# Performance work log

Hardware: AMD Instinct MI355X
Metric: run time of the kernel (lower is better)

The kernel has to match this reference:

```python
import jax, jax.numpy as jnp
import numpy as np

NUM_NODES = 50000
NUM_EDGES = 800000
IN_CH = 128
OUT_CH = 128


def setup_inputs() -> dict:
    key = jax.random.key(0)
    k1, k2, k3 = jax.random.split(key, 3)
    x = jax.random.normal(k1, (NUM_NODES, IN_CH), dtype=jnp.float32)
    # xavier_uniform-like init for weight
    limit = float(np.sqrt(6.0 / (IN_CH + OUT_CH)))
    weight = jax.random.uniform(k2, (IN_CH, OUT_CH), dtype=jnp.float32, minval=-limit, maxval=limit)
    edge_index = jax.random.randint(k3, (2, NUM_EDGES), 0, NUM_NODES, dtype=jnp.int64)
    return {"x": x, "weight": weight, "edge_index": edge_index}


def reference(x, weight, edge_index):
    # GCN-style layer: out = D^{-1/2} A D^{-1/2} x W, with A built from COO edges
    # (duplicate edges sum, matching torch sparse_coo_tensor coalescing).
    num_nodes = x.shape[0]
    row, col = edge_index[0], edge_index[1]
    ones = jnp.ones(edge_index.shape[1], dtype=x.dtype)
    deg = jax.ops.segment_sum(ones, row, num_segments=num_nodes)  # row-sum of A
    deg = jnp.where(deg == 0, jnp.asarray(1.0, x.dtype), deg)
    dinv = deg ** -0.5  # [N]
    coef = dinv[row] * dinv[col]  # per-edge normalized value [E]
    msgs = x[col] * coef[:, None]  # gather + scale, [E, C_in]
    agg = jax.ops.segment_sum(msgs, row, num_segments=num_nodes)  # scatter-add, [N, C_in]
    return agg @ weight  # [N, C_out]
```

## Files before the change

kernel.cpp:

```cpp
#include <hip/hip_runtime.h>

#define N_NODES 50000
#define N_EDGES 800000
#define CH 128
#define SLOT 64
#define NB ((N_NODES + 255) / 256)
#define CAP 5120
#define SUB 4
#define RPB 64
#define FBLK 782
#define GRID (FBLK * 2)

typedef __attribute__((ext_vector_type(8))) short bf16x8;
typedef __attribute__((ext_vector_type(4))) float f32x4;

static __device__ inline unsigned f2bf(float f) {
    union { float f; unsigned u; } v; v.f = f;
    unsigned r = v.u + 0x7fff + ((v.u >> 16) & 1);
    return r >> 16;
}
static __device__ inline float bflo(unsigned v) { union { unsigned u; float f; } c; c.u = v << 16; return c.f; }
static __device__ inline float bfhi(unsigned v) { union { unsigned u; float f; } c; c.u = v & 0xffff0000u; return c.f; }

__global__ __launch_bounds__(256) void k_prep(const float* __restrict__ W,
                                              unsigned short* __restrict__ wT,
                                              int* __restrict__ bcur) {
    int t = blockIdx.x * 256 + threadIdx.x;
    if (t < NB) bcur[t] = 0;
    if (t < CH * CH) {
        int n = t >> 7, k = t & 127;
        wT[t] = (unsigned short)f2bf(W[k * CH + n]);
    }
}

__global__ __launch_bounds__(256) void k_fgA(const int* __restrict__ rowv,
                                             const int* __restrict__ colv,
                                             const float* __restrict__ x,
                                             const unsigned short* __restrict__ wT,
                                             int* __restrict__ bcur,
                                             unsigned* __restrict__ pedges,
                                             unsigned short* __restrict__ yh) {
    __shared__ int hist[NB];
    __shared__ int base[NB];
    int gidx = blockIdx.x;
    int t = threadIdx.x;

    if (!(gidx & 1)) {
        int e0 = (gidx >> 1) * 1024 + t;
        int r[4], c[4], b[4], lr[4];
        bool v[4];
        if (t < NB) hist[t] = 0;
        __syncthreads();
        #pragma unroll
        for (int j = 0; j < 4; ++j) {
            int e = e0 + j * 256;
            v[j] = e < N_EDGES;
            if (v[j]) { r[j] = rowv[e]; c[j] = colv[e]; b[j] = r[j] >> 8; }
        }
        #pragma unroll
        for (int j = 0; j < 4; ++j)
            if (v[j]) lr[j] = atomicAdd(&hist[b[j]], 1);
        __syncthreads();
        if (t < NB) {
            int n = hist[t];
            base[t] = n ? atomicAdd(&bcur[t], n) : 0;
        }
        __syncthreads();
        #pragma unroll
        for (int j = 0; j < 4; ++j) {
            if (v[j]) {
                int pos = base[b[j]] + lr[j];
                if (pos < CAP)
                    pedges[(size_t)b[j] * CAP + pos] = ((unsigned)(r[j] & 255) << 16) | (unsigned)c[j];
            }
        }
        return;
    }

    int row0 = (gidx >> 1) * 64;
    int lane = t & 63, w = t >> 6;
    int m = lane & 15, q = lane >> 4;

    int row = row0 + 16 * w + m;
    int rc = row < N_NODES ? row : N_NODES - 1;
    const float4* xr = (const float4*)(x + (size_t)rc * CH);
    bf16x8 afr[4];
    #pragma unroll
    for (int kk = 0; kk < 4; ++kk) {
        float4 a0 = xr[kk * 8 + q * 2];
        float4 a1 = xr[kk * 8 + q * 2 + 1];
        bf16x8 a;
        a[0] = (short)f2bf(a0.x); a[1] = (short)f2bf(a0.y);
        a[2] = (short)f2bf(a0.z); a[3] = (short)f2bf(a0.w);
        a[4] = (short)f2bf(a1.x); a[5] = (short)f2bf(a1.y);
        a[6] = (short)f2bf(a1.z); a[7] = (short)f2bf(a1.w);
        afr[kk] = a;
    }

    f32x4 acc[8];
    #pragma unroll
    for (int c = 0; c < 8; ++c) acc[c] = (f32x4){0.f, 0.f, 0.f, 0.f};

    #pragma unroll
    for (int c = 0; c < 8; ++c) {
        int n = c * 16 + m;
        const bf16x8* wrow = (const bf16x8*)(wT + (size_t)n * CH);
        #pragma unroll
        for (int kk = 0; kk < 4; ++kk)
            acc[c] = __builtin_amdgcn_mfma_f32_16x16x32_bf16(afr[kk], wrow[kk * 4 + q], acc[c], 0, 0, 0);
    }

    #pragma unroll
    for (int c = 0; c < 8; ++c) {
        #pragma unroll
        for (int r = 0; r < 4; ++r) {
            int orow = row0 + 16 * w + q * 4 + r;
            if (orow < N_NODES)
                yh[(size_t)orow * CH + c * 16 + m] = (unsigned short)f2bf(acc[c][r]);
        }
    }
}

__global__ __launch_bounds__(256) void k_build(const int* __restrict__ bcur,
                                               const unsigned* __restrict__ pedges,
                                               unsigned short* __restrict__ csrP,
                                               int* __restrict__ deg,
                                               float* __restrict__ dinv) {
    __shared__ unsigned short bins[RPB][SLOT];
    __shared__ int rcnt[RPB];
    int b = blockIdx.x / SUB;
    int s = blockIdx.x % SUB;
    int t = threadIdx.x;
    if (t < RPB) rcnt[t] = 0;
    __syncthreads();

    int cnt = bcur[b];
    if (cnt > CAP) cnt = CAP;
    const unsigned* pe = pedges + (size_t)b * CAP;
    for (int i = t; i < cnt; i += 256) {
        unsigned u = pe[i];
        int rlo = u >> 16;
        if ((rlo >> 6) == s) {
            int p = atomicAdd(&rcnt[rlo & 63], 1);
            if (p < SLOT) bins[rlo & 63][p] = (unsigned short)(u & 0xffff);
        }
    }
    __syncthreads();

    int row0 = b * 256 + s * RPB;
    if (t < RPB) {
        int row = row0 + t;
        if (row < N_NODES) {
            int d = rcnt[t];
            deg[row] = d;
            dinv[row] = rsqrtf((float)(d > 0 ? d : 1));
        }
    }
    int rmax = N_NODES - row0;
    if (rmax <= 0) return;
    if (rmax > RPB) rmax = RPB;
    uint4* dst = (uint4*)(csrP + (size_t)row0 * SLOT);
    const uint4* src = (const uint4*)bins;
    for (int k = t; k < rmax * 8; k += 256)
        dst[k] = src[k];
}

__global__ __launch_bounds__(256) void k_agg(const int* __restrict__ deg,
                                             const float* __restrict__ dinv,
                                             const unsigned short* __restrict__ csrP,
                                             const unsigned short* __restrict__ yh,
                                             float* __restrict__ out) {
    int gid = blockIdx.x * 256 + threadIdx.x;
    int n = gid >> 6;
    int lane = threadIdx.x & 63;
    if (n >= N_NODES) return;
    int d = deg[n];
    int cnt = d < SLOT ? d : SLOT;
    float dr = dinv[n];
    const unsigned* __restrict__ y2 = (const unsigned*)yh;
    const uint4* __restrict__ crow = (const uint4*)(csrP + (size_t)n * SLOT);
    float ax = 0.f, ay = 0.f;
    int j = 0;
    for (; j + 16 <= cnt; j += 16) {
        uint4 ca = crow[j >> 3];
        uint4 cb = crow[(j >> 3) + 1];
        int c_[16];
        c_[0] = ca.x & 0xffff;  c_[1] = ca.x >> 16;
        c_[2] = ca.y & 0xffff;  c_[3] = ca.y >> 16;
        c_[4] = ca.z & 0xffff;  c_[5] = ca.z >> 16;
        c_[6] = ca.w & 0xffff;  c_[7] = ca.w >> 16;
        c_[8] = cb.x & 0xffff;  c_[9] = cb.x >> 16;
        c_[10] = cb.y & 0xffff; c_[11] = cb.y >> 16;
        c_[12] = cb.z & 0xffff; c_[13] = cb.z >> 16;
        c_[14] = cb.w & 0xffff; c_[15] = cb.w >> 16;
        unsigned v_[16];
        #pragma unroll
        for (int u = 0; u < 16; ++u) v_[u] = y2[c_[u] * 64 + lane];
        float w_[16];
        #pragma unroll
        for (int u = 0; u < 16; ++u) w_[u] = dinv[c_[u]];
        #pragma unroll
        for (int u = 0; u < 16; ++u) {
            ax = fmaf(bflo(v_[u]), w_[u], ax);
            ay = fmaf(bfhi(v_[u]), w_[u], ay);
        }
    }
    for (; j + 8 <= cnt; j += 8) {
        uint4 cc = crow[j >> 3];
        int c0 = cc.x & 0xffff, c1 = cc.x >> 16;
        int c2 = cc.y & 0xffff, c3 = cc.y >> 16;
        int c4 = cc.z & 0xffff, c5 = cc.z >> 16;
        int c6 = cc.w & 0xffff, c7 = cc.w >> 16;
        unsigned v0 = y2[c0 * 64 + lane];
        unsigned v1 = y2[c1 * 64 + lane];
        unsigned v2 = y2[c2 * 64 + lane];
        unsigned v3 = y2[c3 * 64 + lane];
        unsigned v4 = y2[c4 * 64 + lane];
        unsigned v5 = y2[c5 * 64 + lane];
        unsigned v6 = y2[c6 * 64 + lane];
        unsigned v7 = y2[c7 * 64 + lane];
        float w0 = dinv[c0], w1 = dinv[c1], w2 = dinv[c2], w3 = dinv[c3];
        float w4 = dinv[c4], w5 = dinv[c5], w6 = dinv[c6], w7 = dinv[c7];
        ax = fmaf(bflo(v0), w0, ax); ay = fmaf(bfhi(v0), w0, ay);
        ax = fmaf(bflo(v1), w1, ax); ay = fmaf(bfhi(v1), w1, ay);
        ax = fmaf(bflo(v2), w2, ax); ay = fmaf(bfhi(v2), w2, ay);
        ax = fmaf(bflo(v3), w3, ax); ay = fmaf(bfhi(v3), w3, ay);
        ax = fmaf(bflo(v4), w4, ax); ay = fmaf(bfhi(v4), w4, ay);
        ax = fmaf(bflo(v5), w5, ax); ay = fmaf(bfhi(v5), w5, ay);
        ax = fmaf(bflo(v6), w6, ax); ay = fmaf(bfhi(v6), w6, ay);
        ax = fmaf(bflo(v7), w7, ax); ay = fmaf(bfhi(v7), w7, ay);
    }
    for (; j < cnt; ++j) {
        int c = csrP[(size_t)n * SLOT + j];
        float wc = dinv[c];
        unsigned v = y2[c * 64 + lane];
        ax = fmaf(bflo(v), wc, ax); ay = fmaf(bfhi(v), wc, ay);
    }
    ((float2*)out)[n * 64 + lane] = make_float2(ax * dr, ay * dr);
}

extern "C" void kernel_launch(void* const* d_in, const int* in_sizes, int n_in,
                              void* d_out, int out_size, void* d_ws, size_t ws_size,
                              hipStream_t stream) {
    const float* x = (const float*)d_in[0];
    const float* W = (const float*)d_in[1];
    const int* edge = (const int*)d_in[2];
    const int* rowv = edge;
    const int* colv = edge + N_EDGES;
    float* out = (float*)d_out;

    char* p = (char*)d_ws;
    int* bcur = (int*)p;                           p += 1024;
    unsigned* pedges = (unsigned*)p;               p += (size_t)NB * CAP * 4;
    unsigned short* csrP = (unsigned short*)p;     p += (size_t)N_NODES * SLOT * 2;
    unsigned short* yh = (unsigned short*)p;       p += (size_t)N_NODES * CH * 2;
    int* deg = (int*)p;                            p += (size_t)N_NODES * 4;
    float* dinv = (float*)p;                       p += (size_t)N_NODES * 4;
    unsigned short* wT = (unsigned short*)p;

    k_prep <<<64, 256, 0, stream>>>(W, wT, bcur);
    k_fgA  <<<GRID, 256, 0, stream>>>(rowv, colv, x, wT, bcur, pedges, yh);
    k_build<<<NB * SUB, 256, 0, stream>>>(bcur, pedges, csrP, deg, dinv);
    k_agg  <<<(N_NODES * 64 + 255) / 256, 256, 0, stream>>>(deg, dinv, csrP, yh, out);
}
```

Measured before the change: 159.7 us.

## Replace atomic bucket append with per-block fixed-slot partitioned edge staging

Edge binning blocks now handle 4096 edges each and stage them in shared memory per bucket, then write each bucket's slice to a fixed per-(bucket, block) slot region with a count. This removes the global atomic bucket cursor and its zero-init in the prep kernel. The build kernel walks the per-block slices with a one-ahead prefetch instead of reading a contiguous bucket. Each bucket is capped at 64 edges per block; exceeding that would silently drop edges. The larger scattered pedges layout also adds more global reads in the build kernel.

```diff
diff --git a/kernel.cpp b/kernel.cpp
--- a/kernel.cpp
+++ b/kernel.cpp
@@ -4,12 +4,13 @@
 #define N_EDGES 800000
 #define CH 128
 #define SLOT 64
-#define NB ((N_NODES + 255) / 256)
-#define CAP 5120
+#define NB 196
+#define FBLK 196
+#define EPB 4096
+#define SCAP 64
 #define SUB 4
 #define RPB 64
-#define FBLK 782
-#define GRID (FBLK * 2)
+#define GRID (FBLK + 782)
 
 typedef __attribute__((ext_vector_type(8))) short bf16x8;
 typedef __attribute__((ext_vector_type(4))) float f32x4;
@@ -23,10 +24,8 @@
 static __device__ inline float bfhi(unsigned v) { union { unsigned u; float f; } c; c.u = v & 0xffff0000u; return c.f; }
 
 __global__ __launch_bounds__(256) void k_prep(const float* __restrict__ W,
-                                              unsigned short* __restrict__ wT,
-                                              int* __restrict__ bcur) {
+                                              unsigned short* __restrict__ wT) {
     int t = blockIdx.x * 256 + threadIdx.x;
-    if (t < NB) bcur[t] = 0;
     if (t < CH * CH) {
         int n = t >> 7, k = t & 127;
         wT[t] = (unsigned short)f2bf(W[k * CH + n]);
@@ -37,47 +36,53 @@
                                              const int* __restrict__ colv,
                                              const float* __restrict__ x,
                                              const unsigned short* __restrict__ wT,
-                                             int* __restrict__ bcur,
                                              unsigned* __restrict__ pedges,
+                                             int* __restrict__ cnts,
                                              unsigned short* __restrict__ yh) {
-    __shared__ int hist[NB];
-    __shared__ int base[NB];
+    __shared__ unsigned stage[NB * SCAP];
+    __shared__ int scnt[NB];
     int gidx = blockIdx.x;
     int t = threadIdx.x;
 
-    if (!(gidx & 1)) {
-        int e0 = (gidx >> 1) * 1024 + t;
-        int r[4], c[4], b[4], lr[4];
-        bool v[4];
-        if (t < NB) hist[t] = 0;
+    if (gidx % 5 == 0) {
+        int fbid = gidx / 5;
+        int e0 = fbid * EPB + t;
+        int r_[16], c_[16];
+        #pragma unroll
+        for (int j = 0; j < 16; ++j) {
+            int e = e0 + j * 256;
+            bool v = e < N_EDGES;
+            r_[j] = v ? rowv[e] : -1;
+            c_[j] = v ? colv[e] : 0;
+        }
+        if (t < NB) scnt[t] = 0;
         __syncthreads();
         #pragma unroll
-        for (int j = 0; j < 4; ++j) {
-            int e = e0 + j * 256;
-            v[j] = e < N_EDGES;
-            if (v[j]) { r[j] = rowv[e]; c[j] = colv[e]; b[j] = r[j] >> 8; }
-        }
-        #pragma unroll
-        for (int j = 0; j < 4; ++j)
-            if (v[j]) lr[j] = atomicAdd(&hist[b[j]], 1);
+        for (int j = 0; j < 16; ++j) {
+            if (r_[j] >= 0) {
+                int b = r_[j] >> 8;
+                int p = atomicAdd(&scnt[b], 1);
+                if (p < SCAP)
+                    stage[b * SCAP + ((p + b) & (SCAP - 1))] =
+                        ((unsigned)(r_[j] & 255) << 16) | (unsigned)c_[j];
+            }
+        }
         __syncthreads();
+        int w = t >> 6, ln = t & 63;
+        for (int b = w * 49; b < w * 49 + 49; ++b) {
+            int cnt = scnt[b]; if (cnt > SCAP) cnt = SCAP;
+            if (ln < cnt)
+                pedges[((size_t)b * FBLK + fbid) * SCAP + ln] =
+                    stage[b * SCAP + (((ln) + b) & (SCAP - 1))];
+        }
         if (t < NB) {
-            int n = hist[t];
-            base[t] = n ? atomicAdd(&bcur[t], n) : 0;
-        }
-        __syncthreads();
-        #pragma unroll
-        for (int j = 0; j < 4; ++j) {
-            if (v[j]) {
-                int pos = base[b[j]] + lr[j];
-                if (pos < CAP)
-                    pedges[(size_t)b[j] * CAP + pos] = ((unsigned)(r[j] & 255) << 16) | (unsigned)c[j];
-            }
+            int cnt = scnt[t]; if (cnt > SCAP) cnt = SCAP;
+            cnts[(size_t)fbid * NB + t] = cnt;
         }
         return;
     }
 
-    int row0 = (gidx >> 1) * 64;
+    int row0 = (gidx - (gidx + 4) / 5) * 64;
     int lane = t & 63, w = t >> 6;
     int m = lane & 15, q = lane >> 4;
 
@@ -121,28 +126,42 @@
     }
 }
 
-__global__ __launch_bounds__(256) void k_build(const int* __restrict__ bcur,
+__global__ __launch_bounds__(256) void k_build(const int* __restrict__ cnts,
                                                const unsigned* __restrict__ pedges,
                                                unsigned short* __restrict__ csrP,
                                                int* __restrict__ deg,
                                                float* __restrict__ dinv) {
     __shared__ unsigned short bins[RPB][SLOT];
     __shared__ int rcnt[RPB];
-    int b = blockIdx.x / SUB;
-    int s = blockIdx.x % SUB;
+    int b = blockIdx.x >> 2;
+    int s = blockIdx.x & 3;
     int t = threadIdx.x;
+    int w = t >> 6, ln = t & 63;
     if (t < RPB) rcnt[t] = 0;
     __syncthreads();
 
-    int cnt = bcur[b];
-    if (cnt > CAP) cnt = CAP;
-    const unsigned* pe = pedges + (size_t)b * CAP;
-    for (int i = t; i < cnt; i += 256) {
-        unsigned u = pe[i];
-        int rlo = u >> 16;
+    const unsigned NOEDGE = 0xffffffffu;
+    int fb = w;
+    int cnt0 = cnts[(size_t)fb * NB + b];
+    unsigned u0 = (ln < cnt0) ? pedges[((size_t)b * FBLK + fb) * SCAP + ln] : NOEDGE;
+    for (; fb + 4 < FBLK; ) {
+        int fb1 = fb + 4;
+        int cnt1 = cnts[(size_t)fb1 * NB + b];
+        unsigned u1 = (ln < cnt1) ? pedges[((size_t)b * FBLK + fb1) * SCAP + ln] : NOEDGE;
+        if (u0 != NOEDGE) {
+            int rlo = u0 >> 16;
+            if ((rlo >> 6) == s) {
+                int p = atomicAdd(&rcnt[rlo & 63], 1);
+                if (p < SLOT) bins[rlo & 63][p] = (unsigned short)(u0 & 0xffff);
+            }
+        }
+        u0 = u1; fb = fb1;
+    }
+    if (u0 != NOEDGE) {
+        int rlo = u0 >> 16;
         if ((rlo >> 6) == s) {
             int p = atomicAdd(&rcnt[rlo & 63], 1);
-            if (p < SLOT) bins[rlo & 63][p] = (unsigned short)(u & 0xffff);
+            if (p < SLOT) bins[rlo & 63][p] = (unsigned short)(u0 & 0xffff);
         }
     }
     __syncthreads();
@@ -250,16 +269,16 @@
     float* out = (float*)d_out;
 
     char* p = (char*)d_ws;
-    int* bcur = (int*)p;                           p += 1024;
-    unsigned* pedges = (unsigned*)p;               p += (size_t)NB * CAP * 4;
+    unsigned* pedges = (unsigned*)p;               p += (size_t)NB * FBLK * SCAP * 4;
+    int* cnts = (int*)p;                           p += (size_t)FBLK * NB * 4;
     unsigned short* csrP = (unsigned short*)p;     p += (size_t)N_NODES * SLOT * 2;
     unsigned short* yh = (unsigned short*)p;       p += (size_t)N_NODES * CH * 2;
     int* deg = (int*)p;                            p += (size_t)N_NODES * 4;
     float* dinv = (float*)p;                       p += (size_t)N_NODES * 4;
     unsigned short* wT = (unsigned short*)p;
 
-    k_prep <<<64, 256, 0, stream>>>(W, wT, bcur);
-    k_fgA  <<<GRID, 256, 0, stream>>>(rowv, colv, x, wT, bcur, pedges, yh);
-    k_build<<<NB * SUB, 256, 0, stream>>>(bcur, pedges, csrP, deg, dinv);
+    k_prep <<<64, 256, 0, stream>>>(W, wT);
+    k_fgA  <<<GRID, 256, 0, stream>>>(rowv, colv, x, wT, pedges, cnts, yh);
+    k_build<<<NB * SUB, 256, 0, stream>>>(cnts, pedges, csrP, deg, dinv);
     k_agg  <<<(N_NODES * 64 + 255) / 256, 256, 0, stream>>>(deg, dinv, csrP, yh, out);
 }
```

After: 162.6 us. About the same (+1.8%).
